# Performance work log

Measured on AMD Instinct MI355X. Metric: run time of the kernel, lower is better.

The kernel has to match this reference:

```python
import jax, jax.numpy as jnp
import numpy as np

TOP_K = 2  # Router hardcodes torch.topk(logits, k=2)


def setup_inputs() -> dict:
    key = jax.random.key(0)
    ks = jax.random.split(key, 5)
    B, S, H, I, E = 2, 2048, 1024, 2816, 8
    x = jax.random.normal(ks[0], (B, S, H), dtype=jnp.float32)
    router_w = jax.random.normal(ks[1], (E, H), dtype=jnp.float32) * (1.0 / np.sqrt(H))
    Wg = jax.random.normal(ks[2], (E, I, H), dtype=jnp.float32) * (1.0 / np.sqrt(H))
    Wu = jax.random.normal(ks[3], (E, I, H), dtype=jnp.float32) * (1.0 / np.sqrt(H))
    Wd = jax.random.normal(ks[4], (E, H, I), dtype=jnp.float32) * (1.0 / np.sqrt(I))
    return {"x": x, "router_w": router_w, "Wg": Wg, "Wu": Wu, "Wd": Wd}


def reference(x, router_w, Wg, Wu, Wd):
    B, S, H = x.shape
    E = router_w.shape[0]
    xf = x.reshape(-1, H)  # [T, H], T = B*S

    # Router: logits -> top-2 -> softmax over the selected 2 logits
    logits = xf @ router_w.T                      # [T, E]
    top_vals, top_idx = jax.lax.top_k(logits, TOP_K)  # [T, 2]
    top_w = jax.nn.softmax(top_vals, axis=-1)     # [T, 2]

    # Dense combine weights: combine[t, e] = sum_k top_w[t,k] * (top_idx[t,k] == e)
    combine = jnp.einsum('tke,tk->te', jax.nn.one_hot(top_idx, E, dtype=xf.dtype), top_w)  # [T, E]

    # All-experts SwiGLU FFN (dense grouped GEMM form, eval: dropout is identity)
    g = jnp.einsum('th,eih->eti', xf, Wg)         # [E, T, I]
    u = jnp.einsum('th,eih->eti', xf, Wu)         # [E, T, I]
    h = jax.nn.silu(g) * u                        # [E, T, I]
    y = jnp.einsum('eti,ehi->eth', h, Wd)         # [E, T, H]

    out = jnp.einsum('te,eth->th', combine, y)    # [T, H]
    return out.reshape(B, S, H)
```

## Files before the change

### kernel.cpp

```cpp
#include <hip/hip_runtime.h>
#include <hip/hip_bf16.h>
#include <stdint.h>

#define T_TOK 4096
#define H_DIM 1024
#define I_DIM 2816
#define E_NUM 8
#define BK 64
#define W_ELEMS 23068672
#define CH4 5632
#define NG1 (8 * 44 * 32)

typedef float f32x4 __attribute__((ext_vector_type(4)));
typedef __bf16 bf16x8 __attribute__((ext_vector_type(8)));
typedef __bf16 bf16x4 __attribute__((ext_vector_type(4)));

__device__ __forceinline__ void gload_lds16(const void* g, void* l) {
    __builtin_amdgcn_global_load_lds((const __attribute__((address_space(1))) void*)g,
                                     (__attribute__((address_space(3))) void*)l, 16, 0, 0);
}

__device__ __forceinline__ bf16x8 cvt8(float4 a, float4 b) {
    bf16x8 r;
    r[0] = (__bf16)a.x; r[1] = (__bf16)a.y; r[2] = (__bf16)a.z; r[3] = (__bf16)a.w;
    r[4] = (__bf16)b.x; r[5] = (__bf16)b.y; r[6] = (__bf16)b.z; r[7] = (__bf16)b.w;
    return r;
}

__device__ __forceinline__ bf16x4 cvt4(float4 v) {
    bf16x4 o;
    o[0] = (__bf16)v.x; o[1] = (__bf16)v.y; o[2] = (__bf16)v.z; o[3] = (__bf16)v.w;
    return o;
}

__global__ __launch_bounds__(256) void k_cvt(const float* __restrict__ src,
                                             __bf16* __restrict__ dst, int n8) {
    const int gsz = gridDim.x * 256;
    const float4* s = (const float4*)src;
    int p = blockIdx.x * 256 + threadIdx.x;
    for (; p + gsz < n8; p += 2 * gsz) {
        float4 a0 = s[2 * p], a1 = s[2 * p + 1];
        int q = p + gsz;
        float4 b0 = s[2 * q], b1 = s[2 * q + 1];
        ((bf16x8*)dst)[p] = cvt8(a0, a1);
        ((bf16x8*)dst)[q] = cvt8(b0, b1);
    }
    if (p < n8) {
        float4 a0 = s[2 * p], a1 = s[2 * p + 1];
        ((bf16x8*)dst)[p] = cvt8(a0, a1);
    }
}

__device__ __forceinline__ void cvt_chunk4(const float* __restrict__ src,
                                           __bf16* __restrict__ dst, int chunk, int tid) {
    int i = chunk * 1024 + tid * 4;
    float4 v0 = ((const float4*)src)[i];
    float4 v1 = ((const float4*)src)[i + 1];
    float4 v2 = ((const float4*)src)[i + 2];
    float4 v3 = ((const float4*)src)[i + 3];
    ((bf16x8*)dst)[chunk * 512 + tid * 2]     = cvt8(v0, v1);
    ((bf16x8*)dst)[chunk * 512 + tid * 2 + 1] = cvt8(v2, v3);
}

__global__ __launch_bounds__(256) void k_router(const float* __restrict__ x,
                                                const float* __restrict__ rw,
                                                __bf16* __restrict__ xbf,
                                                int* __restrict__ tops,
                                                float* __restrict__ wslot) {
    const int tid = threadIdx.x;
    const int wid = tid >> 6, lane = tid & 63;
    const int t = blockIdx.x * 4 + wid;

    float acc[E_NUM];
#pragma unroll
    for (int e = 0; e < E_NUM; ++e) acc[e] = 0.f;

    const float4* x4 = (const float4*)(x + (size_t)t * H_DIM);
    const float4* r4 = (const float4*)rw;
#pragma unroll
    for (int j = 0; j < 4; ++j) {
        float4 xv = x4[j * 64 + lane];
        ((bf16x4*)xbf)[(size_t)t * 256 + j * 64 + lane] = cvt4(xv);
#pragma unroll
        for (int e = 0; e < E_NUM; ++e) {
            float4 wv = r4[e * 256 + j * 64 + lane];
            acc[e] += xv.x * wv.x + xv.y * wv.y + xv.z * wv.z + xv.w * wv.w;
        }
    }
#pragma unroll
    for (int s = 1; s < 64; s <<= 1) {
#pragma unroll
        for (int e = 0; e < E_NUM; ++e) acc[e] += __shfl_xor(acc[e], s, 64);
    }
    if (lane == 0) {
        float best = -1e30f; int be = 0;
#pragma unroll
        for (int e = 0; e < E_NUM; ++e) if (acc[e] > best) { best = acc[e]; be = e; }
        float sec = -1e30f; int se = 0;
#pragma unroll
        for (int e = 0; e < E_NUM; ++e) if (e != be && acc[e] > sec) { sec = acc[e]; se = e; }
        float d = __expf(sec - best);
        tops[t] = be | (se << 8);
        wslot[2 * t] = 1.f / (1.f + d);
        wslot[2 * t + 1] = d / (1.f + d);
    }
}

__global__ __launch_bounds__(64) void k_build(const int* __restrict__ tops,
                                              int* __restrict__ list,
                                              int* __restrict__ counts) {
    const int lane = threadIdx.x;
    const unsigned long long ltmask = (1ull << lane) - 1;
    int cnt[E_NUM];
#pragma unroll
    for (int e = 0; e < E_NUM; ++e) cnt[e] = 0;

    for (int i = 0; i < T_TOK / 64; ++i) {
        int t = i * 64 + lane;
        int p = tops[t];
        int e1 = p & 255, e2 = (p >> 8) & 255;
#pragma unroll
        for (int e = 0; e < E_NUM; ++e) {
            unsigned long long m1 = __ballot(e1 == e);
            if (e1 == e)
                list[e * T_TOK + cnt[e] + __popcll(m1 & ltmask)] = 2 * t;
            int tot1 = __popcll(m1);
            unsigned long long m2 = __ballot(e2 == e);
            if (e2 == e)
                list[e * T_TOK + cnt[e] + tot1 + __popcll(m2 & ltmask)] = 2 * t + 1;
            cnt[e] += tot1 + __popcll(m2);
        }
    }
    if (lane == 0) {
#pragma unroll
        for (int e = 0; e < E_NUM; ++e) counts[e] = cnt[e];
    }
}

__global__ __launch_bounds__(256, 4) void k_gemm1(const __bf16* __restrict__ xbf,
                                                  const __bf16* __restrict__ wbf,
                                                  const float* __restrict__ Wd,
                                                  __bf16* __restrict__ wd_bf,
                                                  const int* __restrict__ list,
                                                  const int* __restrict__ counts,
                                                  __bf16* __restrict__ hbuf) {
    __shared__ __attribute__((aligned(16))) unsigned char lA[128 * 128];
    __shared__ __attribute__((aligned(16))) unsigned char lBg[64 * 128];
    __shared__ __attribute__((aligned(16))) unsigned char lBu[64 * 128];
    __shared__ int slots[128];

    const int lid = blockIdx.x;
    const int tid = threadIdx.x;
    if (lid >= NG1) {
        cvt_chunk4(Wd, wd_bf, lid - NG1, tid);
        return;
    }

    const __bf16* wg = wbf;
    const __bf16* wu = wbf + (size_t)W_ELEMS;

    const int e = lid & 7;
    const int seq = lid >> 3;
    const int tn = seq >> 5;
    const int tm = seq & 31;
    const int cnt = counts[e];
    if (tm * 128 >= cnt) return;
    const int lane = tid & 63;
    const int wid = tid >> 6;
    const int wm = wid >> 1;
    const int wn = wid & 1;

    if (tid < 128) {
        int p = tm * 128 + tid;
        slots[tid] = list[e * T_TOK + (p < cnt ? p : cnt - 1)];
    }
    __syncthreads();

    const char* aSrc[4];
    uint32_t aOff[4];
    {
        int colb = (tid & 7) * 16;
#pragma unroll
        for (int r = 0; r < 4; ++r) {
            int row = r * 32 + (tid >> 3);
            int tok = slots[row] >> 1;
            aSrc[r] = (const char*)xbf + (size_t)tok * (H_DIM * 2) + (colb ^ ((row & 7) << 4));
            aOff[r] = (uint32_t)(row * 128 + colb);
        }
    }
    const char* bgSrc[2];
    const char* buSrc[2];
    uint32_t bOff[2];
    {
        int colb = (tid & 7) * 16;
#pragma unroll
        for (int r = 0; r < 2; ++r) {
            int row = r * 32 + (tid >> 3);
            size_t gr = ((size_t)e * I_DIM + (size_t)tn * 64 + row) * (H_DIM * 2) + (colb ^ ((row & 7) << 4));
            bgSrc[r] = (const char*)wg + gr;
            buSrc[r] = (const char*)wu + gr;
            bOff[r] = (uint32_t)(row * 128 + colb);
        }
    }

    const f32x4 zero = {0.f, 0.f, 0.f, 0.f};
    f32x4 accg[4][2], accu[4][2];
#pragma unroll
    for (int i = 0; i < 4; ++i)
#pragma unroll
        for (int j = 0; j < 2; ++j) { accg[i][j] = zero; accu[i][j] = zero; }

    const int NT = H_DIM / BK;
    for (int kt = 0; kt < NT; ++kt) {
        if (kt > 0) __syncthreads();
#pragma unroll
        for (int r = 0; r < 4; ++r) gload_lds16(aSrc[r] + kt * 128, &lA[aOff[r]]);
#pragma unroll
        for (int r = 0; r < 2; ++r) {
            gload_lds16(bgSrc[r] + kt * 128, &lBg[bOff[r]]);
            gload_lds16(buSrc[r] + kt * 128, &lBu[bOff[r]]);
        }
        __syncthreads();
        __builtin_amdgcn_s_setprio(1);
#pragma unroll
        for (int kk = 0; kk < 2; ++kk) {
            bf16x8 av[4], bg[2], bu[2];
#pragma unroll
            for (int mi = 0; mi < 4; ++mi) {
                int row = wm * 64 + mi * 16 + (lane & 15);
                int byte = (row * 128 + kk * 64 + (lane >> 4) * 16) ^ ((row & 7) << 4);
                av[mi] = *(const bf16x8*)&lA[byte];
            }
#pragma unroll
            for (int ni = 0; ni < 2; ++ni) {
                int row = wn * 32 + ni * 16 + (lane & 15);
                int byte = (row * 128 + kk * 64 + (lane >> 4) * 16) ^ ((row & 7) << 4);
                bg[ni] = *(const bf16x8*)&lBg[byte];
                bu[ni] = *(const bf16x8*)&lBu[byte];
            }
#pragma unroll
            for (int mi = 0; mi < 4; ++mi)
#pragma unroll
                for (int ni = 0; ni < 2; ++ni) {
                    accg[mi][ni] = __builtin_amdgcn_mfma_f32_16x16x32_bf16(av[mi], bg[ni], accg[mi][ni], 0, 0, 0);
                    accu[mi][ni] = __builtin_amdgcn_mfma_f32_16x16x32_bf16(av[mi], bu[ni], accu[mi][ni], 0, 0, 0);
                }
        }
        __builtin_amdgcn_s_setprio(0);
    }

#pragma unroll
    for (int mi = 0; mi < 4; ++mi) {
#pragma unroll
        for (int ni = 0; ni < 2; ++ni) {
            int col = tn * 64 + wn * 32 + ni * 16 + (lane & 15);
#pragma unroll
            for (int r = 0; r < 4; ++r) {
                int trow = wm * 64 + mi * 16 + ((lane >> 4) << 2) + r;
                if (tm * 128 + trow < cnt) {
                    float g = accg[mi][ni][r];
                    float u = accu[mi][ni][r];
                    float hv = (g / (1.f + __expf(-g))) * u;
                    hbuf[(size_t)slots[trow] * I_DIM + col] = (__bf16)hv;
                }
            }
        }
    }
}

__global__ __launch_bounds__(256, 4) void k_gemm2(const __bf16* __restrict__ hbuf,
                                                  const __bf16* __restrict__ wd,
                                                  const int* __restrict__ list,
                                                  const int* __restrict__ counts,
                                                  const float* __restrict__ wslot,
                                                  float* __restrict__ out) {
    __shared__ __attribute__((aligned(16))) unsigned char lA[128 * 128];
    __shared__ __attribute__((aligned(16))) unsigned char lB[128 * 128];
    __shared__ int slots[128];
    __shared__ float wr[128];

    const int lid = blockIdx.x;
    const int e = lid & 7;
    const int seq = lid >> 3;
    const int tn = seq & 7;
    const int kh = (seq >> 3) & 1;
    const int tm = seq >> 4;
    const int cnt = counts[e];
    if (tm * 128 >= cnt) return;
    const int tid = threadIdx.x;
    const int lane = tid & 63;
    const int wid = tid >> 6;
    const int wm = wid >> 1;
    const int wn = wid & 1;

    if (tid < 128) {
        int p = tm * 128 + tid;
        int sl = list[e * T_TOK + (p < cnt ? p : cnt - 1)];
        slots[tid] = sl;
        wr[tid] = wslot[sl];
    }
    __syncthreads();

    const int NTH = (I_DIM / BK) / 2;
    const int kbase = kh * NTH;

    const char* aSrc[4];
    uint32_t aOff[4];
    {
        int colb = (tid & 7) * 16;
#pragma unroll
        for (int r = 0; r < 4; ++r) {
            int row = r * 32 + (tid >> 3);
            aSrc[r] = (const char*)hbuf + (size_t)slots[row] * (I_DIM * 2)
                      + (size_t)kbase * 128 + (colb ^ ((row & 7) << 4));
            aOff[r] = (uint32_t)(row * 128 + colb);
        }
    }
    const char* bSrc[4];
    uint32_t bOff[4];
    {
        int colb = (tid & 7) * 16;
#pragma unroll
        for (int r = 0; r < 4; ++r) {
            int row = r * 32 + (tid >> 3);
            bSrc[r] = (const char*)wd + ((size_t)e * H_DIM + (size_t)tn * 128 + row) * (I_DIM * 2)
                      + (size_t)kbase * 128 + (colb ^ ((row & 7) << 4));
            bOff[r] = (uint32_t)(row * 128 + colb);
        }
    }

    const f32x4 zero = {0.f, 0.f, 0.f, 0.f};
    f32x4 acc[4][4];
#pragma unroll
    for (int i = 0; i < 4; ++i)
#pragma unroll
        for (int j = 0; j < 4; ++j) acc[i][j] = zero;

    for (int kt = 0; kt < NTH; ++kt) {
        if (kt > 0) __syncthreads();
#pragma unroll
        for (int r = 0; r < 4; ++r) {
            gload_lds16(aSrc[r] + kt * 128, &lA[aOff[r]]);
            gload_lds16(bSrc[r] + kt * 128, &lB[bOff[r]]);
        }
        __syncthreads();
        __builtin_amdgcn_s_setprio(1);
#pragma unroll
        for (int kk = 0; kk < 2; ++kk) {
            bf16x8 av[4], bv[4];
#pragma unroll
            for (int mi = 0; mi < 4; ++mi) {
                int row = wm * 64 + mi * 16 + (lane & 15);
                int byte = (row * 128 + kk * 64 + (lane >> 4) * 16) ^ ((row & 7) << 4);
                av[mi] = *(const bf16x8*)&lA[byte];
            }
#pragma unroll
            for (int ni = 0; ni < 4; ++ni) {
                int row = wn * 64 + ni * 16 + (lane & 15);
                int byte = (row * 128 + kk * 64 + (lane >> 4) * 16) ^ ((row & 7) << 4);
                bv[ni] = *(const bf16x8*)&lB[byte];
            }
#pragma unroll
            for (int mi = 0; mi < 4; ++mi)
#pragma unroll
                for (int ni = 0; ni < 4; ++ni)
                    acc[mi][ni] = __builtin_amdgcn_mfma_f32_16x16x32_bf16(av[mi], bv[ni], acc[mi][ni], 0, 0, 0);
        }
        __builtin_amdgcn_s_setprio(0);
    }

#pragma unroll
    for (int mi = 0; mi < 4; ++mi) {
#pragma unroll
        for (int ni = 0; ni < 4; ++ni) {
            int col = tn * 128 + wn * 64 + ni * 16 + (lane & 15);
#pragma unroll
            for (int r = 0; r < 4; ++r) {
                int trow = wm * 64 + mi * 16 + ((lane >> 4) << 2) + r;
                if (tm * 128 + trow < cnt) {
                    int t = slots[trow] >> 1;
                    atomicAdd(out + (size_t)t * H_DIM + col, acc[mi][ni][r] * wr[trow]);
                }
            }
        }
    }
}

extern "C" void kernel_launch(void* const* d_in, const int* in_sizes, int n_in,
                              void* d_out, int out_size, void* d_ws, size_t ws_size,
                              hipStream_t stream) {
    const float* x  = (const float*)d_in[0];
    const float* rw = (const float*)d_in[1];
    const float* Wg = (const float*)d_in[2];
    const float* Wu = (const float*)d_in[3];
    const float* Wd = (const float*)d_in[4];
    float* out = (float*)d_out;

    char* ws = (char*)d_ws;
    const size_t SZ_X = 8388608;
    const size_t SZ_W = 46137344;
    __bf16* xbf   = (__bf16*)(ws);
    __bf16* wbf   = (__bf16*)(ws + SZ_X);
    __bf16* wd_bf = (__bf16*)(ws + SZ_X + 2 * SZ_W);
    __bf16* hbuf  = (__bf16*)(ws + SZ_X + 3 * SZ_W);
    int*    tops  = (int*)hbuf;
    int*    list  = (int*)(ws + SZ_X + 4 * SZ_W);
    float*  wslot = (float*)(ws + SZ_X + 4 * SZ_W + 131072);
    int*    counts= (int*)(ws + SZ_X + 4 * SZ_W + 131072 + 32768);

    hipMemsetAsync(d_out, 0, (size_t)out_size * sizeof(float), stream);

    k_router<<<T_TOK / 4, 256, 0, stream>>>(x, rw, xbf, tops, wslot);
    k_build<<<1, 64, 0, stream>>>(tops, list, counts);
    k_cvt<<<2048, 256, 0, stream>>>(Wg, wbf, W_ELEMS / 8);
    k_cvt<<<2048, 256, 0, stream>>>(Wu, wbf + (size_t)W_ELEMS, W_ELEMS / 8);
    k_gemm1<<<NG1 + CH4, 256, 0, stream>>>(xbf, wbf, Wd, wd_bf, list, counts, hbuf);
    k_gemm2<<<8 * 8 * 2 * 32, 256, 0, stream>>>(hbuf, wd_bf, list, counts, wslot, out);
}
```

Baseline: 371.7 us.

## Fuse router with weight conversion, parallelize list build, replace atomics with combine pass

Router and the two Wg/Wu fp32-to-bf16 conversions are merged into one launch, and the expert list build runs one wavefront per expert instead of a single wavefront looping over all experts. The down-projection now writes per-slot, per-K-half partial outputs to a workspace buffer (reusing the no-longer-needed wbf region) instead of doing weighted atomicAdds into the output. A new combine kernel then sums the two halves for both slots and applies the routing weights. This also removes the output memset. In exchange it adds an extra write and read of a large fp32 intermediate.

```diff
diff --git a/kernel.cpp b/kernel.cpp
--- a/kernel.cpp
+++ b/kernel.cpp
@@ -33,11 +33,12 @@
     return o;
 }
 
-__global__ __launch_bounds__(256) void k_cvt(const float* __restrict__ src,
-                                             __bf16* __restrict__ dst, int n8) {
-    const int gsz = gridDim.x * 256;
+__device__ __forceinline__ void cvt_stride(const float* __restrict__ src,
+                                           __bf16* __restrict__ dst, int bb, int tid) {
+    const int n8 = W_ELEMS / 8;
+    const int gsz = 2048 * 256;
     const float4* s = (const float4*)src;
-    int p = blockIdx.x * 256 + threadIdx.x;
+    int p = bb * 256 + tid;
     for (; p + gsz < n8; p += 2 * gsz) {
         float4 a0 = s[2 * p], a1 = s[2 * p + 1];
         int q = p + gsz;
@@ -62,14 +63,22 @@
     ((bf16x8*)dst)[chunk * 512 + tid * 2 + 1] = cvt8(v2, v3);
 }
 
-__global__ __launch_bounds__(256) void k_router(const float* __restrict__ x,
-                                                const float* __restrict__ rw,
-                                                __bf16* __restrict__ xbf,
-                                                int* __restrict__ tops,
-                                                float* __restrict__ wslot) {
+__global__ __launch_bounds__(256) void k_prep(const float* __restrict__ x,
+                                              const float* __restrict__ rw,
+                                              const float* __restrict__ Wg,
+                                              const float* __restrict__ Wu,
+                                              __bf16* __restrict__ xbf,
+                                              __bf16* __restrict__ wbf,
+                                              int* __restrict__ tops,
+                                              float* __restrict__ wslot) {
+    const int b = blockIdx.x;
     const int tid = threadIdx.x;
+    if (b < 2048) { cvt_stride(Wg, wbf, b, tid); return; }
+    if (b < 4096) { cvt_stride(Wu, wbf + (size_t)W_ELEMS, b - 2048, tid); return; }
+
+    const int rb = b - 4096;
     const int wid = tid >> 6, lane = tid & 63;
-    const int t = blockIdx.x * 4 + wid;
+    const int t = rb * 4 + wid;
 
     float acc[E_NUM];
 #pragma unroll
@@ -109,32 +118,24 @@
 __global__ __launch_bounds__(64) void k_build(const int* __restrict__ tops,
                                               int* __restrict__ list,
                                               int* __restrict__ counts) {
+    const int e = blockIdx.x;
     const int lane = threadIdx.x;
     const unsigned long long ltmask = (1ull << lane) - 1;
-    int cnt[E_NUM];
-#pragma unroll
-    for (int e = 0; e < E_NUM; ++e) cnt[e] = 0;
+    int cnt = 0;
 
     for (int i = 0; i < T_TOK / 64; ++i) {
         int t = i * 64 + lane;
         int p = tops[t];
-        int e1 = p & 255, e2 = (p >> 8) & 255;
-#pragma unroll
-        for (int e = 0; e < E_NUM; ++e) {
-            unsigned long long m1 = __ballot(e1 == e);
-            if (e1 == e)
-                list[e * T_TOK + cnt[e] + __popcll(m1 & ltmask)] = 2 * t;
-            int tot1 = __popcll(m1);
-            unsigned long long m2 = __ballot(e2 == e);
-            if (e2 == e)
-                list[e * T_TOK + cnt[e] + tot1 + __popcll(m2 & ltmask)] = 2 * t + 1;
-            cnt[e] += tot1 + __popcll(m2);
-        }
-    }
-    if (lane == 0) {
-#pragma unroll
-        for (int e = 0; e < E_NUM; ++e) counts[e] = cnt[e];
-    }
+        bool h1 = (p & 255) == e;
+        bool h2 = ((p >> 8) & 255) == e;
+        unsigned long long m1 = __ballot(h1);
+        if (h1) list[e * T_TOK + cnt + __popcll(m1 & ltmask)] = 2 * t;
+        int n1 = __popcll(m1);
+        unsigned long long m2 = __ballot(h2);
+        if (h2) list[e * T_TOK + cnt + n1 + __popcll(m2 & ltmask)] = 2 * t + 1;
+        cnt += n1 + __popcll(m2);
+    }
+    if (lane == 0) counts[e] = cnt;
 }
 
 __global__ __launch_bounds__(256, 4) void k_gemm1(const __bf16* __restrict__ xbf,
@@ -272,12 +273,10 @@
                                                   const __bf16* __restrict__ wd,
                                                   const int* __restrict__ list,
                                                   const int* __restrict__ counts,
-                                                  const float* __restrict__ wslot,
-                                                  float* __restrict__ out) {
+                                                  float* __restrict__ y) {
     __shared__ __attribute__((aligned(16))) unsigned char lA[128 * 128];
     __shared__ __attribute__((aligned(16))) unsigned char lB[128 * 128];
     __shared__ int slots[128];
-    __shared__ float wr[128];
 
     const int lid = blockIdx.x;
     const int e = lid & 7;
@@ -295,14 +294,13 @@
 
     if (tid < 128) {
         int p = tm * 128 + tid;
-        int sl = list[e * T_TOK + (p < cnt ? p : cnt - 1)];
-        slots[tid] = sl;
-        wr[tid] = wslot[sl];
+        slots[tid] = list[e * T_TOK + (p < cnt ? p : cnt - 1)];
     }
     __syncthreads();
 
     const int NTH = (I_DIM / BK) / 2;
     const int kbase = kh * NTH;
+    float* yh = y + (size_t)kh * (2 * T_TOK) * H_DIM;
 
     const char* aSrc[4];
     uint32_t aOff[4];
@@ -377,13 +375,32 @@
 #pragma unroll
             for (int r = 0; r < 4; ++r) {
                 int trow = wm * 64 + mi * 16 + ((lane >> 4) << 2) + r;
-                if (tm * 128 + trow < cnt) {
-                    int t = slots[trow] >> 1;
-                    atomicAdd(out + (size_t)t * H_DIM + col, acc[mi][ni][r] * wr[trow]);
-                }
-            }
-        }
-    }
+                if (tm * 128 + trow < cnt)
+                    yh[(size_t)slots[trow] * H_DIM + col] = acc[mi][ni][r];
+            }
+        }
+    }
+}
+
+__global__ __launch_bounds__(256) void k_combine(const float* __restrict__ y,
+                                                 const float* __restrict__ wslot,
+                                                 float* __restrict__ out) {
+    const int t = blockIdx.x;
+    const int c = threadIdx.x;
+    const float w1 = wslot[2 * t];
+    const float w2 = wslot[2 * t + 1];
+    const size_t half = (size_t)(2 * T_TOK) * H_DIM / 4;
+    const float4* y4 = (const float4*)y;
+    size_t r1 = (size_t)(2 * t) * (H_DIM / 4) + c;
+    size_t r2 = (size_t)(2 * t + 1) * (H_DIM / 4) + c;
+    float4 a0 = y4[r1], a1 = y4[r1 + half];
+    float4 b0 = y4[r2], b1 = y4[r2 + half];
+    float4 o;
+    o.x = w1 * (a0.x + a1.x) + w2 * (b0.x + b1.x);
+    o.y = w1 * (a0.y + a1.y) + w2 * (b0.y + b1.y);
+    o.z = w1 * (a0.z + a1.z) + w2 * (b0.z + b1.z);
+    o.w = w1 * (a0.w + a1.w) + w2 * (b0.w + b1.w);
+    ((float4*)out)[(size_t)t * (H_DIM / 4) + c] = o;
 }
 
 extern "C" void kernel_launch(void* const* d_in, const int* in_sizes, int n_in,
@@ -403,17 +420,15 @@
     __bf16* wbf   = (__bf16*)(ws + SZ_X);
     __bf16* wd_bf = (__bf16*)(ws + SZ_X + 2 * SZ_W);
     __bf16* hbuf  = (__bf16*)(ws + SZ_X + 3 * SZ_W);
+    float*  y     = (float*)(ws + SZ_X);
     int*    tops  = (int*)hbuf;
     int*    list  = (int*)(ws + SZ_X + 4 * SZ_W);
     float*  wslot = (float*)(ws + SZ_X + 4 * SZ_W + 131072);
     int*    counts= (int*)(ws + SZ_X + 4 * SZ_W + 131072 + 32768);
 
-    hipMemsetAsync(d_out, 0, (size_t)out_size * sizeof(float), stream);
-
-    k_router<<<T_TOK / 4, 256, 0, stream>>>(x, rw, xbf, tops, wslot);
-    k_build<<<1, 64, 0, stream>>>(tops, list, counts);
-    k_cvt<<<2048, 256, 0, stream>>>(Wg, wbf, W_ELEMS / 8);
-    k_cvt<<<2048, 256, 0, stream>>>(Wu, wbf + (size_t)W_ELEMS, W_ELEMS / 8);
+    k_prep<<<5120, 256, 0, stream>>>(x, rw, Wg, Wu, xbf, wbf, tops, wslot);
+    k_build<<<E_NUM, 64, 0, stream>>>(tops, list, counts);
     k_gemm1<<<NG1 + CH4, 256, 0, stream>>>(xbf, wbf, Wd, wd_bf, list, counts, hbuf);
-    k_gemm2<<<8 * 8 * 2 * 32, 256, 0, stream>>>(hbuf, wd_bf, list, counts, wslot, out);
-}
+    k_gemm2<<<8 * 8 * 2 * 32, 256, 0, stream>>>(hbuf, wd_bf, list, counts, y);
+    k_combine<<<T_TOK, 256, 0, stream>>>(y, wslot, out);
+}
```

Result: faster. 307.3 us (-17.3%).
